# Optimization experiments

Measured on AMD Instinct MI355X. Metric: run time of the kernel, lower is better.

## Reference

```python
import jax, jax.numpy as jnp
import numpy as np

D_MODEL = 1024
D_ATTN = 1024
N_HEADS = 16
D_FF = 4096
EPS = 1e-6


def _ln(x, gamma, beta):
    # Matches the custom LayerNorm: (x - mean) / (std + eps), std = sqrt(biased var)
    mean = jnp.mean(x, axis=-1, keepdims=True)
    std = jnp.sqrt(jnp.mean((x - mean) ** 2, axis=-1, keepdims=True))
    return gamma * ((x - mean) / (std + EPS)) + beta


def setup_inputs() -> dict:
    key = jax.random.key(0)
    ks = jax.random.split(key, 16)
    s = 0.02
    d, da, dff = D_MODEL, D_ATTN, D_FF
    inp = {
        "x": jax.random.normal(ks[0], (1, 2048, d), dtype=jnp.float32),
        "g1": jnp.ones((d,), jnp.float32),
        "beta1": jnp.zeros((d,), jnp.float32),
        "W_in": jax.random.normal(ks[1], (d, da), jnp.float32) * s,
        "b_in": jnp.zeros((da,), jnp.float32),
        "Wq": jax.random.normal(ks[2], (da, da), jnp.float32) * s,
        "bq": jnp.zeros((da,), jnp.float32),
        "Wk": jax.random.normal(ks[3], (da, da), jnp.float32) * s,
        "bk": jnp.zeros((da,), jnp.float32),
        "Wv": jax.random.normal(ks[4], (da, da), jnp.float32) * s,
        "bv": jnp.zeros((da,), jnp.float32),
        "Wo": jax.random.normal(ks[5], (da, da), jnp.float32) * s,
        "bo": jnp.zeros((da,), jnp.float32),
        "W2": jax.random.normal(ks[6], (da, d), jnp.float32) * s,
        "b2": jnp.zeros((d,), jnp.float32),
        "g2": jnp.ones((d,), jnp.float32),
        "beta2": jnp.zeros((d,), jnp.float32),
        "Wf1": jax.random.normal(ks[7], (d, dff), jnp.float32) * s,
        "bf1": jnp.zeros((dff,), jnp.float32),
        "Wf2": jax.random.normal(ks[8], (dff, d), jnp.float32) * s,
        "bf2": jnp.zeros((d,), jnp.float32),
    }
    return inp


def reference(x, g1, beta1, W_in, b_in, Wq, bq, Wk, bk, Wv, bv, Wo, bo,
              W2, b2, g2, beta2, Wf1, bf1, Wf2, bf2):
    B, S, _ = x.shape
    H, dk = N_HEADS, D_ATTN // N_HEADS

    norm_x = _ln(x, g1, beta1)
    h = norm_x @ W_in + b_in                      # [B,S,d_attn]

    def split_heads(t):
        return t.reshape(B, S, H, dk).transpose(0, 2, 1, 3)  # [B,H,S,dk]

    q = split_heads(h @ Wq + bq)
    k = split_heads(h @ Wk + bk)
    v = split_heads(h @ Wv + bv)

    scores = jnp.einsum("bhqd,bhkd->bhqk", q, k) / jnp.sqrt(jnp.float32(dk))
    causal = jnp.tril(jnp.ones((S, S), bool))[None, None]
    scores = jnp.where(causal, scores, -jnp.inf)
    attn_weights = jax.nn.softmax(scores, axis=-1)            # [B,H,S,S]
    ctx = jnp.einsum("bhqk,bhkd->bhqd", attn_weights, v)
    ctx = ctx.transpose(0, 2, 1, 3).reshape(B, S, D_ATTN)
    mha_out = ctx @ Wo + bo

    part1 = x + (mha_out @ W2 + b2)
    norm2 = _ln(part1, g2, beta2)
    ff = jnp.maximum(norm2 @ Wf1 + bf1, 0.0) @ Wf2 + bf2
    out = norm2 + ff
    return out, attn_weights
```

## Files before the change

### kernel.cpp

```cpp
#include <hip/hip_runtime.h>
#include <hip/hip_bf16.h>
#include <cstdint>

#define S_LEN 2048
#define D_MOD 1024
#define N_HEADS 16
#define DK 64
#define D_FF 4096

typedef __bf16 bf16x8 __attribute__((ext_vector_type(8)));
typedef float f32x4 __attribute__((ext_vector_type(4)));

#define MFMA16(a, b, c) __builtin_amdgcn_mfma_f32_16x16x32_bf16((a), (b), (c), 0, 0, 0)

__device__ inline unsigned pack_bf16x2(float a, float b)
{
    unsigned short ua = __builtin_bit_cast(unsigned short, (__bf16)a);
    unsigned short ub = __builtin_bit_cast(unsigned short, (__bf16)b);
    return (unsigned)ua | ((unsigned)ub << 16);
}

__device__ inline void gload16(const void* g, void* l)
{
    __builtin_amdgcn_global_load_lds(
        (const __attribute__((address_space(1))) unsigned int*)g,
        (__attribute__((address_space(3))) unsigned int*)l, 16, 0, 0);
}

template<int BN, bool RELU, bool RES, bool RES2, bool WF32, bool WBF16, bool WVT>
__device__ __forceinline__
void gemm_dev(const __bf16* __restrict__ A, const __bf16* __restrict__ BT,
              const float* __restrict__ bias, const float* __restrict__ res,
              const float* __restrict__ res2,
              float* __restrict__ Cf, __bf16* __restrict__ Cb,
              __bf16* __restrict__ vt,
              int N, int Kst, int Klp, int bx, int by,
              uint4* As, uint4* Bs)
{
    constexpr int NFRAG = BN / 32;
    const int tid = threadIdx.x;
    const int lane = tid & 63;
    const int w = tid >> 6;
    const int lrow = lane & 15;
    const int g = lane >> 4;
    const int bm = by * 128;
    const int bn = bx * BN;
    const int wrow = (w >> 1) * 64;
    const int wcol = (w & 1) * (BN / 2);

    f32x4 acc[4][NFRAG];
    for (int m = 0; m < 4; m++)
        for (int n = 0; n < NFRAG; n++)
            acc[m][n] = (f32x4){0.f, 0.f, 0.f, 0.f};

    const int srow = tid >> 3;
    const int sc = tid & 7;
    const __bf16* Ag = A + (size_t)(bm + srow) * Kst + sc * 8;
    const __bf16* Bg = BT + (size_t)(bn + srow) * Kst + sc * 8;

    auto stage = [&](int kt, int tb) {
        uint4* Ad = As + tb * 128 * 8;
        uint4* Bd = Bs + tb * BN * 8;
        #pragma unroll
        for (int p = 0; p < 4; p++)
            gload16(Ag + (size_t)(p * 32) * Kst + kt, &Ad[(srow + p * 32) * 8 + sc]);
        #pragma unroll
        for (int p = 0; p < NFRAG; p++)
            gload16(Bg + (size_t)(p * 32) * Kst + kt, &Bd[(srow + p * 32) * 8 + sc]);
    };

    stage(0, 0);

    int it = 0;
    for (int kt = 0; kt < Klp; kt += 64, ++it) {
        const int cur = it & 1;
        if (kt + 64 < Klp) {
            stage(kt + 64, cur ^ 1);
            if constexpr (NFRAG == 4)
                asm volatile("s_waitcnt vmcnt(8)" ::: "memory");
            else
                asm volatile("s_waitcnt vmcnt(6)" ::: "memory");
        } else {
            asm volatile("s_waitcnt vmcnt(0)" ::: "memory");
        }
        __syncthreads();
        const uint4* Ab = As + cur * 128 * 8;
        const uint4* Bb = Bs + cur * BN * 8;
        #pragma unroll
        for (int kk = 0; kk < 2; kk++) {
            bf16x8 af[4], bfr[NFRAG];
            int c = kk * 4 + g;
            #pragma unroll
            for (int m = 0; m < 4; m++)
                af[m] = __builtin_bit_cast(bf16x8, Ab[(wrow + m * 16 + lrow) * 8 + c]);
            #pragma unroll
            for (int n = 0; n < NFRAG; n++)
                bfr[n] = __builtin_bit_cast(bf16x8, Bb[(wcol + n * 16 + lrow) * 8 + c]);
            #pragma unroll
            for (int m = 0; m < 4; m++)
                #pragma unroll
                for (int n = 0; n < NFRAG; n++)
                    acc[m][n] = MFMA16(af[m], bfr[n], acc[m][n]);
        }
        __syncthreads();
    }

    for (int n = 0; n < NFRAG; n++) {
        int col = bn + wcol + n * 16 + lrow;
        float bval = bias ? bias[col] : 0.f;
        for (int m = 0; m < 4; m++) {
            int row0 = bm + wrow + m * 16 + g * 4;
            float vv[4];
            for (int r = 0; r < 4; r++) {
                int row = row0 + r;
                float v = acc[m][n][r] + bval;
                if (RELU) v = fmaxf(v, 0.f);
                if (RES) v += res[(size_t)row * N + col];
                if (RES2) v += res2[(size_t)row * N + col];
                vv[r] = v;
                if (WF32) Cf[(size_t)row * N + col] = v;
                if (WBF16) Cb[(size_t)row * N + col] = (__bf16)v;
            }
            if (WVT && col >= 2048) {
                uint2 pk;
                pk.x = pack_bf16x2(vv[0], vv[1]);
                pk.y = pack_bf16x2(vv[2], vv[3]);
                *(uint2*)(vt + (size_t)(col - 2048) * S_LEN + row0) = pk;
            }
        }
    }
}

__device__ __forceinline__
void ln_row_v(int row, float4 v, const float* __restrict__ gamma,
              const float* __restrict__ beta, __bf16* __restrict__ outb,
              float* __restrict__ outf, float* red)
{
    int tid = threadIdx.x;
    float s = v.x + v.y + v.z + v.w;
    float sq = v.x * v.x + v.y * v.y + v.z * v.z + v.w * v.w;
    for (int off = 32; off; off >>= 1) {
        s += __shfl_down(s, off);
        sq += __shfl_down(sq, off);
    }
    int wid = tid >> 6;
    if ((tid & 63) == 0) { red[wid] = s; red[wid + 4] = sq; }
    __syncthreads();
    s = red[0] + red[1] + red[2] + red[3];
    sq = red[4] + red[5] + red[6] + red[7];
    float mean = s * (1.f / D_MOD);
    float var = fmaxf(sq * (1.f / D_MOD) - mean * mean, 0.f);
    float inv = 1.f / (sqrtf(var) + 1e-6f);
    float4 gv = ((const float4*)gamma)[tid];
    float4 bv = ((const float4*)beta)[tid];
    float y0 = gv.x * ((v.x - mean) * inv) + bv.x;
    float y1 = gv.y * ((v.y - mean) * inv) + bv.y;
    float y2 = gv.z * ((v.z - mean) * inv) + bv.z;
    float y3 = gv.w * ((v.w - mean) * inv) + bv.w;
    uint2 pk;
    pk.x = pack_bf16x2(y0, y1);
    pk.y = pack_bf16x2(y2, y3);
    ((uint2*)(outb + (size_t)row * D_MOD))[tid] = pk;
    if (outf) {
        float4 o = {y0, y1, y2, y3};
        ((float4*)(outf + (size_t)row * D_MOD))[tid] = o;
    }
}

__device__ __forceinline__
void ln_row(int row, const float* __restrict__ x, const float* __restrict__ gamma,
            const float* __restrict__ beta, __bf16* __restrict__ outb,
            float* __restrict__ outf, float* red)
{
    float4 v = ((const float4*)(x + (size_t)row * D_MOD))[threadIdx.x];
    ln_row_v(row, v, gamma, beta, outb, outf, red);
}

__device__ __forceinline__
void pwrite_tile(const __bf16* __restrict__ qkv, const float* __restrict__ Obuf,
                 float* __restrict__ P, int h, int qt, int kt)
{
    const int tid = threadIdx.x;
    const int lane = tid & 63;
    const int w = tid >> 6;
    const int lrow = lane & 15;
    const int g = lane >> 4;
    const float c1 = 0.18033688f;
    const __bf16* ksec = qkv + 1024;
    const size_t Pb = (size_t)h * S_LEN * S_LEN;

    bf16x8 qfr[2][2];
    #pragma unroll
    for (int qq = 0; qq < 2; qq++)
        #pragma unroll
        for (int kk = 0; kk < 2; kk++)
            qfr[qq][kk] = *(const bf16x8*)(qkv +
                (size_t)(qt * 128 + w * 32 + qq * 16 + lrow) * 3072 + h * DK + kk * 32 + g * 8);

    f32x4 acc[2][8];
    #pragma unroll
    for (int qq = 0; qq < 2; qq++)
        #pragma unroll
        for (int mf = 0; mf < 8; mf++) acc[qq][mf] = (f32x4){0.f, 0.f, 0.f, 0.f};
    #pragma unroll
    for (int kk = 0; kk < 2; kk++) {
        #pragma unroll
        for (int mf = 0; mf < 8; mf++) {
            bf16x8 kf = *(const bf16x8*)(ksec +
                (size_t)(kt * 128 + mf * 16 + lrow) * 3072 + h * DK + kk * 32 + g * 8);
            acc[0][mf] = MFMA16(kf, qfr[0][kk], acc[0][mf]);
            acc[1][mf] = MFMA16(kf, qfr[1][kk], acc[1][mf]);
        }
    }

    #pragma unroll
    for (int qq = 0; qq < 2; qq++) {
        int q = qt * 128 + w * 32 + qq * 16 + lrow;
        float offv = Obuf[h * S_LEN + q];
        float* prow = P + Pb + (size_t)q * S_LEN;
        if (kt == qt) {
            #pragma unroll
            for (int mf = 0; mf < 8; mf++) {
                int kvb = kt * 128 + mf * 16 + g * 4;
                f32x4 st;
                st[0] = (kvb + 0 <= q) ? exp2f(acc[qq][mf][0] * c1 + offv) : 0.f;
                st[1] = (kvb + 1 <= q) ? exp2f(acc[qq][mf][1] * c1 + offv) : 0.f;
                st[2] = (kvb + 2 <= q) ? exp2f(acc[qq][mf][2] * c1 + offv) : 0.f;
                st[3] = (kvb + 3 <= q) ? exp2f(acc[qq][mf][3] * c1 + offv) : 0.f;
                __builtin_nontemporal_store(st, (f32x4*)(prow + kvb));
            }
        } else {
            #pragma unroll
            for (int mf = 0; mf < 8; mf++) {
                int kvb = kt * 128 + mf * 16 + g * 4;
                f32x4 st;
                st[0] = exp2f(acc[qq][mf][0] * c1 + offv);
                st[1] = exp2f(acc[qq][mf][1] * c1 + offv);
                st[2] = exp2f(acc[qq][mf][2] * c1 + offv);
                st[3] = exp2f(acc[qq][mf][3] * c1 + offv);
                __builtin_nontemporal_store(st, (f32x4*)(prow + kvb));
            }
        }
    }
}

__device__ __forceinline__
void zfill_tile(float* __restrict__ P, int zid)
{
    int tid = threadIdx.x;
    int h = zid / 120;
    int pr = zid - h * 120;
    int qt = 0, acc = 0;
    while (pr >= acc + 15 - qt) { acc += 15 - qt; qt++; }
    int kt = qt + 1 + (pr - acc);
    f32x4 z = {0.f, 0.f, 0.f, 0.f};
    float* base = P + (size_t)h * S_LEN * S_LEN + (size_t)(qt * 128) * S_LEN + kt * 128;
    #pragma unroll
    for (int i = 0; i < 16; i++) {
        int idx = i * 256 + tid;
        int row = idx >> 5, c = idx & 31;
        __builtin_nontemporal_store(z, (f32x4*)(base + (size_t)row * S_LEN + c * 4));
    }
}

__global__ __launch_bounds__(256)
void prep1(const float* __restrict__ Wq, const float* __restrict__ Wk,
           const float* __restrict__ Wv, const float* __restrict__ W2,
           const float* __restrict__ Wf1, const float* __restrict__ Wf2,
           const float* __restrict__ W_in, const float* __restrict__ Wo,
           const float* __restrict__ b_in, const float* __restrict__ bo,
           __bf16* __restrict__ WqkvT, __bf16* __restrict__ W2T,
           __bf16* __restrict__ Wf1T, __bf16* __restrict__ Wf2T,
           __bf16* __restrict__ Win_b, __bf16* __restrict__ Wo_b,
           float* __restrict__ part)
{
    __shared__ float tile[32][33];
    int id = blockIdx.x;
    int tid = threadIdx.x;
    if (id < 12288) {
        const float* W; __bf16* WT; int K, N, n0, k0;
        if (id < 4096) {
            int m = id >> 10; id &= 1023;
            K = 1024; N = 1024;
            n0 = (id & 31) * 32; k0 = (id >> 5) * 32;
            W = m == 0 ? Wq : (m == 1 ? Wk : (m == 2 ? Wv : W2));
            WT = m == 3 ? W2T : WqkvT + (size_t)m * 1024 * 1024;
        } else if (id < 8192) {
            id -= 4096;
            K = 1024; N = 4096;
            n0 = (id & 127) * 32; k0 = (id >> 7) * 32;
            W = Wf1; WT = Wf1T;
        } else {
            id -= 8192;
            K = 4096; N = 1024;
            n0 = (id & 31) * 32; k0 = (id >> 5) * 32;
            W = Wf2; WT = Wf2T;
        }
        int tx = tid & 31, ty = tid >> 5;
        for (int i = 0; i < 4; i++)
            tile[ty + i * 8][tx] = W[(size_t)(k0 + ty + i * 8) * N + n0 + tx];
        __syncthreads();
        for (int i = 0; i < 4; i++)
            WT[(size_t)(n0 + ty + i * 8) * K + k0 + tx] = (__bf16)tile[tx][ty + i * 8];
        return;
    }
    id -= 12288;
    if (id < 2048) {
        const float* W = id < 1024 ? W_in : Wo;
        __bf16* o = id < 1024 ? Win_b : Wo_b;
        int i = (id & 1023) * 256 + tid;
        float4 v = ((const float4*)W)[i];
        uint2 pk;
        pk.x = pack_bf16x2(v.x, v.y);
        pk.y = pack_bf16x2(v.z, v.w);
        ((uint2*)o)[i] = pk;
        return;
    }
    id -= 2048;
    {
        int n = (id & 15) * 256 + tid;
        int kc = id >> 4;
        int sel = n >> 10, col = n & 1023;
        const float* W = sel == 0 ? Wq : (sel == 1 ? Wk : (sel == 2 ? Wv : W2));
        const float* src = sel < 3 ? b_in : bo;
        float s = 0.f;
        for (int k = kc * 128; k < kc * 128 + 128; k++)
            s += src[k] * W[(size_t)k * 1024 + col];
        part[kc * 4096 + n] = s;
    }
}

__global__ __launch_bounds__(256, 2)
void prep2(const __bf16* __restrict__ WqkvT, const __bf16* __restrict__ Win_b,
           __bf16* __restrict__ WqkvCT,
           const __bf16* __restrict__ W2T, const __bf16* __restrict__ Wo_b,
           __bf16* __restrict__ WcombT,
           const float* __restrict__ part,
           const float* __restrict__ bq, const float* __restrict__ bk,
           const float* __restrict__ bv, const float* __restrict__ b2,
           float* __restrict__ bqkv, float* __restrict__ bcomb,
           const float* __restrict__ x, const float* __restrict__ g1,
           const float* __restrict__ beta1, __bf16* __restrict__ xn_b)
{
    __shared__ uint4 As[2 * 128 * 8];
    __shared__ uint4 Bs[2 * 64 * 8];
    int id = blockIdx.x;
    int tid = threadIdx.x;
    if (id < 384) {
        gemm_dev<64, false, false, false, false, true, false>(
            WqkvT, Win_b, nullptr, nullptr, nullptr, nullptr, WqkvCT, nullptr,
            1024, 1024, 1024, id & 15, id >> 4, As, Bs);
        return;
    }
    id -= 384;
    if (id < 128) {
        gemm_dev<64, false, false, false, false, true, false>(
            W2T, Wo_b, nullptr, nullptr, nullptr, nullptr, WcombT, nullptr,
            1024, 1024, 1024, id & 15, id >> 4, As, Bs);
        return;
    }
    id -= 128;
    if (id < 16) {
        int n = id * 256 + tid;
        int sel = n >> 10, col = n & 1023;
        float s = sel == 0 ? bq[col] : (sel == 1 ? bk[col] : (sel == 2 ? bv[col] : b2[col]));
        for (int kc = 0; kc < 8; kc++) s += part[kc * 4096 + n];
        if (n < 3072) bqkv[n] = s; else bcomb[col] = s;
        return;
    }
    id -= 16;
    ln_row(id, x, g1, beta1, xn_b, nullptr, (float*)As);
}

__global__ __launch_bounds__(256, 2)
void qkv_zf(const __bf16* __restrict__ xn_b, const __bf16* __restrict__ WqkvCT,
            const float* __restrict__ bqkv, __bf16* __restrict__ qkv_b,
            __bf16* __restrict__ vt, float* __restrict__ P)
{
    __shared__ uint4 As[2 * 128 * 8];
    __shared__ uint4 Bs[2 * 128 * 8];
    if (blockIdx.x < 384) {
        int bid = blockIdx.x;
        gemm_dev<128, false, false, false, false, true, true>(
            xn_b, WqkvCT, bqkv, nullptr, nullptr, nullptr, qkv_b, vt,
            3072, 1024, 1024, bid % 24, bid / 24, As, Bs);
        return;
    }
    zfill_tile(P, blockIdx.x - 384);
}

__global__ __launch_bounds__(256, 2)
void part1_split(const __bf16* __restrict__ ctx_b, const __bf16* __restrict__ WcombT,
                 float* __restrict__ pA, float* __restrict__ pB)
{
    __shared__ uint4 As[2 * 128 * 8];
    __shared__ uint4 Bs[2 * 64 * 8];
    int half = blockIdx.x >> 8;
    int b2 = blockIdx.x & 255;
    const __bf16* Ah = ctx_b + half * 512;
    const __bf16* Bh = WcombT + half * 512;
    float* Cf = half ? pB : pA;
    gemm_dev<64, false, false, false, true, false, false>(
        Ah, Bh, nullptr, nullptr, nullptr, Cf, nullptr, nullptr,
        1024, 1024, 512, b2 & 15, b2 >> 4, As, Bs);
}

__global__ __launch_bounds__(256)
void ln2_fused(const float* __restrict__ pA, const float* __restrict__ pB,
               const float* __restrict__ x, const float* __restrict__ bcomb,
               const float* __restrict__ gamma, const float* __restrict__ beta,
               __bf16* __restrict__ outb, float* __restrict__ outf)
{
    __shared__ float red[8];
    int row = blockIdx.x;
    int tid = threadIdx.x;
    float4 a = ((const float4*)(pA + (size_t)row * D_MOD))[tid];
    float4 b = ((const float4*)(pB + (size_t)row * D_MOD))[tid];
    float4 xv = ((const float4*)(x + (size_t)row * D_MOD))[tid];
    float4 bc = ((const float4*)bcomb)[tid];
    float4 v;
    v.x = a.x + b.x + xv.x + bc.x;
    v.y = a.y + b.y + xv.y + bc.y;
    v.z = a.z + b.z + xv.z + bc.z;
    v.w = a.w + b.w + xv.w + bc.w;
    ln_row_v(row, v, gamma, beta, outb, outf, red);
}

__global__ __launch_bounds__(256, 2)
void attn_flash(const __bf16* __restrict__ qkv, const __bf16* __restrict__ vt,
                float* __restrict__ Obuf, __bf16* __restrict__ ctx,
                float* __restrict__ P)
{
    __shared__ char Ks[2][16384];
    __shared__ char Vs[2][16384];
    __shared__ char Plds[4][4096];
    const int tid = threadIdx.x;

    if (blockIdx.x >= 512) {
        zfill_tile(P, 960 + (int)blockIdx.x - 512);
        return;
    }

    const int lane = tid & 63;
    const int w = tid >> 6;
    const int lrow = lane & 15;
    const int g = lane >> 4;
    const int h = blockIdx.x & 15;
    const int b = 31 - ((int)blockIdx.x >> 4);
    const int qg = b * 64 + w * 16 + lrow;
    const int ntiles = (b >> 1) + 1;
    const float c1 = 0.18033688f;
    const __bf16* ksec = qkv + 1024;
    char* plB = Plds[w];

    bf16x8 qf[2];
    qf[0] = *(const bf16x8*)(qkv + (size_t)qg * 3072 + h * DK + g * 8);
    qf[1] = *(const bf16x8*)(qkv + (size_t)qg * 3072 + h * DK + 32 + g * 8);

    float m2 = -1e30f, l = 0.f;
    f32x4 acc2[4];
    #pragma unroll
    for (int i = 0; i < 4; i++) acc2[i] = (f32x4){0.f, 0.f, 0.f, 0.f};

    const int sKrow = (w << 3) + (lane >> 3);
    const int sKch = lane & 7;
    const int sVrow = (w << 2) + (lane >> 4);
    const int sVch = lane & 15;

    auto stage = [&](int kt, int tb) {
        char* KsW = Ks[tb] + w * 1024;
        char* VsW = Vs[tb] + w * 1024;
        #pragma unroll
        for (int p = 0; p < 4; p++) {
            int row = sKrow + p * 32;
            int ch = sKch ^ (row & 7);
            gload16(ksec + (size_t)(kt * 128 + row) * 3072 + h * DK + ch * 8,
                    KsW + p * 4096 + lane * 16);
        }
        #pragma unroll
        for (int p = 0; p < 4; p++) {
            int row = sVrow + p * 16;
            int ch = sVch ^ (row & 7);
            gload16(vt + (size_t)(h * DK + row) * S_LEN + kt * 128 + ch * 8,
                    VsW + p * 4096 + lane * 16);
        }
    };

    stage(0, 0);

    for (int kt = 0; kt < ntiles; kt++) {
        const int cur = kt & 1;
        if (kt + 1 < ntiles) {
            stage(kt + 1, cur ^ 1);
            asm volatile("s_waitcnt vmcnt(8)" ::: "memory");
        } else {
            asm volatile("s_waitcnt vmcnt(0)" ::: "memory");
        }
        __syncthreads();

        const char* Ksb = Ks[cur];
        const char* Vsb = Vs[cur];

        f32x4 acc[8];
        #pragma unroll
        for (int mf = 0; mf < 8; mf++) acc[mf] = (f32x4){0.f, 0.f, 0.f, 0.f};
        #pragma unroll
        for (int kk = 0; kk < 2; kk++)
            #pragma unroll
            for (int mf = 0; mf < 8; mf++) {
                int row = mf * 16 + lrow;
                bf16x8 kf = *(const bf16x8*)(Ksb + row * 128 + (((kk * 4 + g) ^ (row & 7)) << 4));
                acc[mf] = MFMA16(kf, qf[kk], acc[mf]);
            }

        float s[8][4];
        float tmx = -1e30f;
        const bool lastT = (kt == ntiles - 1);
        #pragma unroll
        for (int mf = 0; mf < 8; mf++) {
            int kvb = kt * 128 + mf * 16 + g * 4;
            #pragma unroll
            for (int r = 0; r < 4; r++) {
                float sv = acc[mf][r] * c1;
                if (lastT) sv = (kvb + r <= qg) ? sv : -1e30f;
                s[mf][r] = sv;
                tmx = fmaxf(tmx, sv);
            }
        }
        if (!__all((int)(tmx <= m2 + 6.f))) {
            float tm = fmaxf(tmx, __shfl_xor(tmx, 16));
            tm = fmaxf(tm, __shfl_xor(tm, 32));
            float nm = fmaxf(m2, tm);
            float sc = exp2f(m2 - nm);
            l *= sc;
            #pragma unroll
            for (int md = 0; md < 4; md++) acc2[md] *= sc;
            m2 = nm;
        }
        float sum = 0.f;
        #pragma unroll
        for (int mf = 0; mf < 8; mf++) {
            float p0 = exp2f(s[mf][0] - m2);
            float p1 = exp2f(s[mf][1] - m2);
            float p2 = exp2f(s[mf][2] - m2);
            float p3 = exp2f(s[mf][3] - m2);
            sum += (p0 + p1) + (p2 + p3);
            uint2 pk;
            pk.x = pack_bf16x2(p0, p1);
            pk.y = pack_bf16x2(p2, p3);
            *(uint2*)(plB + ((lrow * 256 + mf * 32 + g * 8) ^ ((lrow & 7) << 4))) = pk;
        }
        l += sum;

        #pragma unroll
        for (int ks = 0; ks < 4; ks++) {
            bf16x8 pf = *(bf16x8*)(plB + ((lrow * 256 + ks * 64 + g * 16) ^ ((lrow & 7) << 4)));
            #pragma unroll
            for (int md = 0; md < 4; md++) {
                int row = md * 16 + lrow;
                bf16x8 vf = *(const bf16x8*)(Vsb + row * 256 + (((ks * 4 + g) ^ (row & 7)) << 4));
                acc2[md] = MFMA16(vf, pf, acc2[md]);
            }
        }
        __syncthreads();
    }

    l += __shfl_xor(l, 16);
    l += __shfl_xor(l, 32);
    float li = 1.f / l;
    if (lane < 16)
        Obuf[h * S_LEN + qg] = -m2 - log2f(l);
    #pragma unroll
    for (int md = 0; md < 4; md++) {
        uint2 pk;
        pk.x = pack_bf16x2(acc2[md][0] * li, acc2[md][1] * li);
        pk.y = pack_bf16x2(acc2[md][2] * li, acc2[md][3] * li);
        *(uint2*)(ctx + (size_t)qg * D_MOD + h * DK + md * 16 + g * 4) = pk;
    }
}

__global__ __launch_bounds__(256, 2)
void ff1_pwrite(const __bf16* __restrict__ A, const __bf16* __restrict__ BT,
                const float* __restrict__ bias, __bf16* __restrict__ Cb,
                const __bf16* __restrict__ qkv, const float* __restrict__ Obuf,
                float* __restrict__ P)
{
    __shared__ uint4 As[2 * 128 * 8];
    __shared__ uint4 Bs[2 * 128 * 8];
    if (blockIdx.x < 512) {
        int bid = blockIdx.x;
        gemm_dev<128, true, false, false, false, true, false>(
            A, BT, bias, nullptr, nullptr, nullptr, Cb, nullptr,
            D_FF, 1024, 1024, bid & 31, bid >> 5, As, Bs);
        return;
    }
    int idp = blockIdx.x - 512;
    int h = idp / 136;
    int tt = idp - h * 136;
    int qt = 0;
    while (tt > qt) { tt -= qt + 1; qt++; }
    pwrite_tile(qkv, Obuf, P, h, qt, tt);
}

__global__ __launch_bounds__(256, 2)
void ff2_pwrite(const __bf16* __restrict__ ff1_b, const __bf16* __restrict__ Wf2T,
                float* __restrict__ partA, float* __restrict__ partB,
                const __bf16* __restrict__ qkv, const float* __restrict__ Obuf,
                float* __restrict__ P)
{
    __shared__ uint4 As[2 * 128 * 8];
    __shared__ uint4 Bs[2 * 64 * 8];
    if (blockIdx.x < 512) {
        int half = blockIdx.x >> 8;
        int b2 = blockIdx.x & 255;
        const __bf16* Ah = ff1_b + half * 2048;
        const __bf16* Bh = Wf2T + half * 2048;
        float* Cf = half ? partB : partA;
        gemm_dev<64, false, false, false, true, false, false>(
            Ah, Bh, nullptr, nullptr, nullptr, Cf, nullptr, nullptr,
            1024, 4096, 2048, b2 & 15, b2 >> 4, As, Bs);
        return;
    }
    int idp = blockIdx.x - 512;
    int h = 8 + idp / 136;
    int tt = idp - (idp / 136) * 136;
    int qt = 0;
    while (tt > qt) { tt -= qt + 1; qt++; }
    pwrite_tile(qkv, Obuf, P, h, qt, tt);
}

__global__ __launch_bounds__(256)
void ff2_reduce(const float* __restrict__ partA, const float* __restrict__ partB,
                const float* __restrict__ norm2f, const float* __restrict__ bf2,
                float* __restrict__ outp)
{
    int idx = blockIdx.x * 256 + threadIdx.x;
    int col = (idx * 4) & 1023;
    f32x4 a = *(const f32x4*)(partA + (size_t)idx * 4);
    f32x4 b = *(const f32x4*)(partB + (size_t)idx * 4);
    f32x4 n = *(const f32x4*)(norm2f + (size_t)idx * 4);
    f32x4 bb = *(const f32x4*)(bf2 + col);
    f32x4 o = a + b + n + bb;
    *(f32x4*)(outp + (size_t)idx * 4) = o;
}

extern "C" void kernel_launch(void* const* d_in, const int* in_sizes, int n_in,
                              void* d_out, int out_size, void* d_ws, size_t ws_size,
                              hipStream_t stream)
{
    const float* x     = (const float*)d_in[0];
    const float* g1    = (const float*)d_in[1];
    const float* beta1 = (const float*)d_in[2];
    const float* W_in  = (const float*)d_in[3];
    const float* b_in  = (const float*)d_in[4];
    const float* Wq    = (const float*)d_in[5];
    const float* bq    = (const float*)d_in[6];
    const float* Wk    = (const float*)d_in[7];
    const float* bk    = (const float*)d_in[8];
    const float* Wv    = (const float*)d_in[9];
    const float* bv    = (const float*)d_in[10];
    const float* Wo    = (const float*)d_in[11];
    const float* bo    = (const float*)d_in[12];
    const float* W2    = (const float*)d_in[13];
    const float* b2    = (const float*)d_in[14];
    const float* g2    = (const float*)d_in[15];
    const float* beta2 = (const float*)d_in[16];
    const float* Wf1   = (const float*)d_in[17];
    const float* bf1   = (const float*)d_in[18];
    const float* Wf2   = (const float*)d_in[19];
    const float* bf2   = (const float*)d_in[20];

    float* outp = (float*)d_out;
    float* Pout = outp + (size_t)S_LEN * D_MOD;

    char* p = (char*)d_ws;
    auto alloc = [&](size_t b) -> void* {
        void* r = (void*)p;
        p += (b + 255) & ~(size_t)255;
        return r;
    };
    __bf16* WqkvT    = (__bf16*)alloc((size_t)3072 * 1024 * 2);
    __bf16* W2T      = (__bf16*)alloc((size_t)1024 * 1024 * 2);
    __bf16* Wf1T     = (__bf16*)alloc((size_t)D_FF * D_MOD * 2);
    __bf16* Wf2T     = (__bf16*)alloc((size_t)D_MOD * D_FF * 2);
    __bf16* WqkvCT   = (__bf16*)alloc((size_t)3072 * 1024 * 2);
    __bf16* WcombT   = (__bf16*)alloc((size_t)1024 * 1024 * 2);
    float*  bqkv     = (float*)alloc((size_t)3072 * 4);
    float*  bcomb    = (float*)alloc((size_t)1024 * 4);
    float*  biaspart = (float*)alloc((size_t)8 * 4096 * 4);
    __bf16* xn_b     = (__bf16*)alloc((size_t)S_LEN * D_MOD * 2);
    __bf16* qkv_b    = (__bf16*)alloc((size_t)S_LEN * 3072 * 2);
    __bf16* VT       = (__bf16*)alloc((size_t)N_HEADS * DK * S_LEN * 2);
    __bf16* ctx_b    = (__bf16*)alloc((size_t)S_LEN * D_MOD * 2);
    float*  part1f   = (float*)alloc((size_t)S_LEN * D_MOD * 4);
    float*  p1B      = (float*)alloc((size_t)S_LEN * D_MOD * 4);
    float*  norm2f   = (float*)alloc((size_t)S_LEN * D_MOD * 4);
    __bf16* norm2b   = (__bf16*)alloc((size_t)S_LEN * D_MOD * 2);
    __bf16* ff1_b    = (__bf16*)alloc((size_t)S_LEN * D_FF * 2);
    float*  Obuf     = (float*)alloc((size_t)N_HEADS * S_LEN * 4);
    float*  ffpartB  = (float*)alloc((size_t)S_LEN * D_MOD * 4);
    __bf16* Win_b   = (__bf16*)part1f;
    __bf16* Wo_b    = (__bf16*)norm2f;
    float*  ffpartA = part1f;

    dim3 blk(256);

    prep1<<<dim3(14464), blk, 0, stream>>>(Wq, Wk, Wv, W2, Wf1, Wf2, W_in, Wo,
                                           b_in, bo, WqkvT, W2T, Wf1T, Wf2T,
                                           Win_b, Wo_b, biaspart);

    prep2<<<dim3(2576), blk, 0, stream>>>(WqkvT, Win_b, WqkvCT, W2T, Wo_b, WcombT,
                                          biaspart, bq, bk, bv, b2, bqkv, bcomb,
                                          x, g1, beta1, xn_b);

    qkv_zf<<<dim3(384 + 960), blk, 0, stream>>>(xn_b, WqkvCT, bqkv, qkv_b, VT, Pout);

    attn_flash<<<dim3(512 + 960), blk, 0, stream>>>(qkv_b, VT, Obuf, ctx_b, Pout);

    part1_split<<<dim3(512), blk, 0, stream>>>(ctx_b, WcombT, part1f, p1B);

    ln2_fused<<<S_LEN, blk, 0, stream>>>(part1f, p1B, x, bcomb, g2, beta2,
                                         norm2b, norm2f);

    ff1_pwrite<<<dim3(512 + 1088), blk, 0, stream>>>(
        norm2b, Wf1T, bf1, ff1_b, qkv_b, Obuf, Pout);

    ff2_pwrite<<<dim3(512 + 1088), blk, 0, stream>>>(
        ff1_b, Wf2T, ffpartA, ffpartB, qkv_b, Obuf, Pout);

    ff2_reduce<<<dim3(2048), blk, 0, stream>>>(ffpartA, ffpartB, norm2f, bf2, outp);
}
```

Baseline: 267.5 us.

## Replace double-buffered GEMM LDS pipeline with single-buffered load-then-compute loop

The shared GEMM device routine no longer prefetches the next K tile into a second LDS buffer while computing the current one. Each iteration now loads straight into a single buffer, waits for all loads, syncs, and computes. All kernel LDS allocations are halved to match. This cuts LDS use, which may let more blocks fit per CU, but global-load latency is no longer hidden behind MFMA work.

After: 252.3 us. -5.7%, faster.

```diff
diff --git a/kernel.cpp b/kernel.cpp
--- a/kernel.cpp
+++ b/kernel.cpp
@@ -58,51 +58,32 @@
     const __bf16* Ag = A + (size_t)(bm + srow) * Kst + sc * 8;
     const __bf16* Bg = BT + (size_t)(bn + srow) * Kst + sc * 8;
 
-    auto stage = [&](int kt, int tb) {
-        uint4* Ad = As + tb * 128 * 8;
-        uint4* Bd = Bs + tb * BN * 8;
+    for (int kt = 0; kt < Klp; kt += 64) {
+        __syncthreads();
         #pragma unroll
         for (int p = 0; p < 4; p++)
-            gload16(Ag + (size_t)(p * 32) * Kst + kt, &Ad[(srow + p * 32) * 8 + sc]);
+            gload16(Ag + (size_t)(p * 32) * Kst + kt, &As[(srow + p * 32) * 8 + sc]);
         #pragma unroll
         for (int p = 0; p < NFRAG; p++)
-            gload16(Bg + (size_t)(p * 32) * Kst + kt, &Bd[(srow + p * 32) * 8 + sc]);
-    };
-
-    stage(0, 0);
-
-    int it = 0;
-    for (int kt = 0; kt < Klp; kt += 64, ++it) {
-        const int cur = it & 1;
-        if (kt + 64 < Klp) {
-            stage(kt + 64, cur ^ 1);
-            if constexpr (NFRAG == 4)
-                asm volatile("s_waitcnt vmcnt(8)" ::: "memory");
-            else
-                asm volatile("s_waitcnt vmcnt(6)" ::: "memory");
-        } else {
-            asm volatile("s_waitcnt vmcnt(0)" ::: "memory");
-        }
+            gload16(Bg + (size_t)(p * 32) * Kst + kt, &Bs[(srow + p * 32) * 8 + sc]);
+        asm volatile("s_waitcnt vmcnt(0)" ::: "memory");
         __syncthreads();
-        const uint4* Ab = As + cur * 128 * 8;
-        const uint4* Bb = Bs + cur * BN * 8;
         #pragma unroll
         for (int kk = 0; kk < 2; kk++) {
             bf16x8 af[4], bfr[NFRAG];
             int c = kk * 4 + g;
             #pragma unroll
             for (int m = 0; m < 4; m++)
-                af[m] = __builtin_bit_cast(bf16x8, Ab[(wrow + m * 16 + lrow) * 8 + c]);
+                af[m] = __builtin_bit_cast(bf16x8, As[(wrow + m * 16 + lrow) * 8 + c]);
             #pragma unroll
             for (int n = 0; n < NFRAG; n++)
-                bfr[n] = __builtin_bit_cast(bf16x8, Bb[(wcol + n * 16 + lrow) * 8 + c]);
+                bfr[n] = __builtin_bit_cast(bf16x8, Bs[(wcol + n * 16 + lrow) * 8 + c]);
             #pragma unroll
             for (int m = 0; m < 4; m++)
                 #pragma unroll
                 for (int n = 0; n < NFRAG; n++)
                     acc[m][n] = MFMA16(af[m], bfr[n], acc[m][n]);
         }
-        __syncthreads();
     }
 
     for (int n = 0; n < NFRAG; n++) {
@@ -342,8 +323,8 @@
            const float* __restrict__ x, const float* __restrict__ g1,
            const float* __restrict__ beta1, __bf16* __restrict__ xn_b)
 {
-    __shared__ uint4 As[2 * 128 * 8];
-    __shared__ uint4 Bs[2 * 64 * 8];
+    __shared__ uint4 As[128 * 8];
+    __shared__ uint4 Bs[64 * 8];
     int id = blockIdx.x;
     int tid = threadIdx.x;
     if (id < 384) {
@@ -377,8 +358,8 @@
             const float* __restrict__ bqkv, __bf16* __restrict__ qkv_b,
             __bf16* __restrict__ vt, float* __restrict__ P)
 {
-    __shared__ uint4 As[2 * 128 * 8];
-    __shared__ uint4 Bs[2 * 128 * 8];
+    __shared__ uint4 As[128 * 8];
+    __shared__ uint4 Bs[128 * 8];
     if (blockIdx.x < 384) {
         int bid = blockIdx.x;
         gemm_dev<128, false, false, false, false, true, true>(
@@ -393,8 +374,8 @@
 void part1_split(const __bf16* __restrict__ ctx_b, const __bf16* __restrict__ WcombT,
                  float* __restrict__ pA, float* __restrict__ pB)
 {
-    __shared__ uint4 As[2 * 128 * 8];
-    __shared__ uint4 Bs[2 * 64 * 8];
+    __shared__ uint4 As[128 * 8];
+    __shared__ uint4 Bs[64 * 8];
     int half = blockIdx.x >> 8;
     int b2 = blockIdx.x & 255;
     const __bf16* Ah = ctx_b + half * 512;
@@ -585,8 +566,8 @@
                 const __bf16* __restrict__ qkv, const float* __restrict__ Obuf,
                 float* __restrict__ P)
 {
-    __shared__ uint4 As[2 * 128 * 8];
-    __shared__ uint4 Bs[2 * 128 * 8];
+    __shared__ uint4 As[128 * 8];
+    __shared__ uint4 Bs[128 * 8];
     if (blockIdx.x < 512) {
         int bid = blockIdx.x;
         gemm_dev<128, true, false, false, false, true, false>(
@@ -608,8 +589,8 @@
                 const __bf16* __restrict__ qkv, const float* __restrict__ Obuf,
                 float* __restrict__ P)
 {
-    __shared__ uint4 As[2 * 128 * 8];
-    __shared__ uint4 Bs[2 * 64 * 8];
+    __shared__ uint4 As[128 * 8];
+    __shared__ uint4 Bs[64 * 8];
     if (blockIdx.x < 512) {
         int half = blockIdx.x >> 8;
         int b2 = blockIdx.x & 255;
```
